# Performance work log

Measured on AMD Instinct MI355X. Metric: run time of the kernel, lower is better.

Reference implementation:

```python
import jax, jax.numpy as jnp
import numpy as np

NUM_HEADS = 12

def _get_rel_pos(q_size, k_size, rel_pos):
    # rel_pos already has shape (2*max(q,k)-1, head_dim) -> no resize needed
    q_coords = jnp.arange(q_size)[:, None] * max(k_size / q_size, 1.0)
    k_coords = jnp.arange(k_size)[None, :] * max(q_size / k_size, 1.0)
    rel = (q_coords - k_coords + (k_size - 1) * max(q_size / k_size, 1.0)).astype(jnp.int32)
    return rel_pos[rel.reshape(-1)].reshape(q_size, k_size, -1)  # (q, k, head_dim)


def setup_inputs() -> dict:
    key = jax.random.key(0)
    ks = jax.random.split(key, 7)
    B, H, W, C = 1, 64, 64, 768
    head_dim = C // NUM_HEADS
    return {
        "x": jax.random.normal(ks[0], (B, H, W, C), jnp.float32),
        "qkv_w": jax.random.normal(ks[1], (C, 3 * C), jnp.float32) * 0.02,
        "qkv_b": jax.random.normal(ks[2], (3 * C,), jnp.float32) * 0.02,
        "rel_pos_h": jax.random.normal(ks[3], (2 * H - 1, head_dim), jnp.float32) * 0.02,
        "rel_pos_w": jax.random.normal(ks[4], (2 * W - 1, head_dim), jnp.float32) * 0.02,
        "proj_w": jax.random.normal(ks[5], (C, C), jnp.float32) * 0.02,
        "proj_b": jax.random.normal(ks[6], (C,), jnp.float32) * 0.02,
    }


def reference(x, qkv_w, qkv_b, rel_pos_h, rel_pos_w, proj_w, proj_b):
    B, H, W, C = x.shape
    nh = NUM_HEADS
    hd = C // nh
    scale = hd ** (-0.5)
    S = H * W

    qkv = x @ qkv_w + qkv_b                              # (B,H,W,3C)
    qkv = qkv.reshape(B, S, 3, nh, hd).transpose(2, 0, 3, 1, 4).reshape(3, B * nh, S, hd)
    q, k, v = qkv[0], qkv[1], qkv[2]                     # (B*nh, S, hd)

    attn = jnp.einsum('bqd,bkd->bqk', q * scale, k)      # (B*nh, S, S)

    rh = _get_rel_pos(H, H, rel_pos_h)                   # (H,H,hd)
    rw = _get_rel_pos(W, W, rel_pos_w)                   # (W,W,hd)
    r_q = q.reshape(B * nh, H, W, hd)
    rel_h = jnp.einsum('bhwc,hkc->bhwk', r_q, rh)        # (B*nh,H,W,H)
    rel_w = jnp.einsum('bhwc,wkc->bhwk', r_q, rw)        # (B*nh,H,W,W)
    attn = (attn.reshape(B * nh, H, W, H, W)
            + rel_h[:, :, :, :, None]
            + rel_w[:, :, :, None, :]).reshape(B * nh, S, S)

    attn = jax.nn.softmax(attn, axis=-1)
    out = jnp.einsum('bqk,bkd->bqd', attn, v)            # (B*nh, S, hd)
    out = out.reshape(B, nh, H, W, hd).transpose(0, 2, 3, 1, 4).reshape(B, H, W, C)
    return out @ proj_w + proj_b
```

## Files before the change

kernel.cpp:

```cpp
#include <hip/hip_runtime.h>
#include <hip/hip_bf16.h>

#define S_TOK 4096
#define CDIM  768
#define N3C   2304
#define NH    12
#define HD    64

#define LOG2E 1.44269504f

typedef __attribute__((ext_vector_type(8))) short short8;
typedef __attribute__((ext_vector_type(4))) short short4v;
typedef __attribute__((ext_vector_type(4))) float float4v;
typedef __attribute__((ext_vector_type(4))) unsigned uint4v;

__device__ __forceinline__ float b2f(short s) {
    return __uint_as_float(((unsigned)(unsigned short)s) << 16);
}
__device__ __forceinline__ short f2b(float f) {
    unsigned u = __float_as_uint(f);
    unsigned r = (u + 0x7FFFu + ((u >> 16) & 1u)) >> 16;
    return (short)r;
}

#if __has_builtin(__builtin_amdgcn_exp2f)
#define EXP2F __builtin_amdgcn_exp2f
#else
#define EXP2F exp2f
#endif

__device__ __forceinline__ unsigned pack_trunc(float a, float b) {
    return __builtin_amdgcn_perm(__float_as_uint(b), __float_as_uint(a), 0x07060302u);
}

__device__ __forceinline__ short8 u4_to_s8(unsigned a, unsigned b, unsigned c, unsigned d) {
    union { uint4v u; short8 s; } t;
    t.u = (uint4v){a, b, c, d};
    return t.s;
}

__global__ __launch_bounds__(256) void cast_bf16_kernel(
    const float* __restrict__ in, short* __restrict__ out, int n4)
{
    int i = blockIdx.x * 256 + threadIdx.x;
    if (i >= n4) return;
    float4 v = ((const float4*)in)[i];
    short4v o4 = { f2b(v.x), f2b(v.y), f2b(v.z), f2b(v.w) };
    *(short4v*)&out[(size_t)i * 4] = o4;
}

__global__ __launch_bounds__(256) void transpose_cast_kernel(
    const float* __restrict__ in, short* __restrict__ out, int R, int C)
{
    __shared__ float t[64][65];
    const int tid = threadIdx.x;
    const int c0 = blockIdx.x * 64, r0 = blockIdx.y * 64;
    const int li = tid >> 6;
    const int lj = tid & 63;
#pragma unroll
    for (int p = 0; p < 16; ++p) {
        int i = p * 4 + li;
        t[i][lj] = in[(size_t)(r0 + i) * C + c0 + lj];
    }
    __syncthreads();
#pragma unroll
    for (int p = 0; p < 16; ++p) {
        int i = p * 4 + li;
        out[(size_t)(c0 + i) * R + r0 + lj] = f2b(t[lj][i]);
    }
}

#define GEMM_CORE(A_, Bt_)                                                     \
    __shared__ __align__(16) short a_s[128][72];                               \
    __shared__ __align__(16) short b_s[128][72];                               \
    const int tid  = threadIdx.x;                                              \
    const int m0 = blockIdx.y * 128;                                           \
    const int n0 = blockIdx.x * 128;                                           \
    const int lane = tid & 63, w = tid >> 6;                                   \
    const int l15 = lane & 15, quad = lane >> 4;                               \
    const int wr = w >> 1, wc = w & 1;                                         \
    const int srow = tid >> 1;                                                 \
    const int scol = (tid & 1) * 32;                                           \
    float4v acc[4][4];                                                         \
    _Pragma("unroll")                                                          \
    for (int i = 0; i < 4; ++i)                                                \
        _Pragma("unroll")                                                      \
        for (int j = 0; j < 4; ++j) acc[i][j] = (float4v){0.f,0.f,0.f,0.f};    \
    for (int k0 = 0; k0 < 768; k0 += 64) {                                     \
        __syncthreads();                                                       \
        const short* ga = A_ + (size_t)(m0 + srow) * 768 + k0 + scol;          \
        const short* gb = Bt_ + (size_t)(n0 + srow) * 768 + k0 + scol;         \
        _Pragma("unroll")                                                      \
        for (int v = 0; v < 4; ++v) {                                          \
            *(uint4*)&a_s[srow][scol + v*8] = *(const uint4*)(ga + v*8);       \
            *(uint4*)&b_s[srow][scol + v*8] = *(const uint4*)(gb + v*8);       \
        }                                                                      \
        __syncthreads();                                                       \
        _Pragma("unroll")                                                      \
        for (int kk = 0; kk < 64; kk += 32) {                                  \
            short8 af[4], bfr[4];                                              \
            _Pragma("unroll")                                                  \
            for (int i = 0; i < 4; ++i)                                        \
                af[i] = *(const short8*)&a_s[wr*64 + i*16 + l15][kk + quad*8]; \
            _Pragma("unroll")                                                  \
            for (int j = 0; j < 4; ++j)                                        \
                bfr[j] = *(const short8*)&b_s[wc*64 + j*16 + l15][kk + quad*8];\
            _Pragma("unroll")                                                  \
            for (int i = 0; i < 4; ++i)                                        \
                _Pragma("unroll")                                              \
                for (int j = 0; j < 4; ++j)                                    \
                    acc[i][j] = __builtin_amdgcn_mfma_f32_16x16x32_bf16(       \
                        af[i], bfr[j], acc[i][j], 0, 0, 0);                    \
        }                                                                      \
    }

__global__ __launch_bounds__(256) void gemm_qkv_mfma(
    const short* __restrict__ A, const short* __restrict__ Bt,
    const float* __restrict__ bias,
    short* __restrict__ Qb, short* __restrict__ Kb, short* __restrict__ Vt)
{
    GEMM_CORE(A, Bt)

    const int sec = n0 / CDIM;
    float bj[4];
#pragma unroll
    for (int j = 0; j < 4; ++j) bj[j] = bias[n0 + wc*64 + j*16 + l15];

    if (sec < 2) {
        short* dst = (sec == 0) ? Qb : Kb;
#pragma unroll
        for (int i = 0; i < 4; ++i)
#pragma unroll
            for (int j = 0; j < 4; ++j) {
                const int nn = (n0 + wc*64 + j*16 + l15) % CDIM;
                const int head = nn >> 6, d = nn & 63;
#pragma unroll
                for (int r = 0; r < 4; ++r) {
                    const int s = m0 + wr*64 + i*16 + quad*4 + r;
                    dst[((size_t)head * S_TOK + s) * HD + d] = f2b(acc[i][j][r] + bj[j]);
                }
            }
    } else {
#pragma unroll
        for (int i = 0; i < 4; ++i)
#pragma unroll
            for (int j = 0; j < 4; ++j) {
                const int nn = (n0 + wc*64 + j*16 + l15) % CDIM;
                const int head = nn >> 6, d = nn & 63;
                const int sbase = m0 + wr*64 + i*16 + quad*4;
                short4v v4;
#pragma unroll
                for (int r = 0; r < 4; ++r) v4[r] = f2b(acc[i][j][r] + bj[j]);
                *(short4v*)&Vt[((size_t)head * HD + d) * S_TOK + sbase] = v4;
            }
    }
}

__global__ __launch_bounds__(256) void gemm_proj_mfma(
    const short* __restrict__ A, const short* __restrict__ Bt,
    const float* __restrict__ bias, float* __restrict__ out)
{
    GEMM_CORE(A, Bt)

    float bj[4];
#pragma unroll
    for (int j = 0; j < 4; ++j) bj[j] = bias[n0 + wc*64 + j*16 + l15];

#pragma unroll
    for (int i = 0; i < 4; ++i)
#pragma unroll
        for (int j = 0; j < 4; ++j) {
            const int n = n0 + wc*64 + j*16 + l15;
#pragma unroll
            for (int r = 0; r < 4; ++r) {
                const int s = m0 + wr*64 + i*16 + quad*4 + r;
                out[(size_t)s * CDIM + n] = acc[i][j][r] + bj[j];
            }
        }
}

__global__ __launch_bounds__(256) void rel_mfma_kernel(
    const short* __restrict__ Qb, const float* __restrict__ rph,
    const float* __restrict__ rpw, short* __restrict__ Relh,
    short* __restrict__ Relw)
{
    __shared__ __align__(16) short q_s [64][72];
    __shared__ __align__(16) short rh_s[64][72];
    __shared__ __align__(16) short rw_s[128][72];

    const int tid  = threadIdx.x;
    const int y    = blockIdx.x;
    const int head = blockIdx.y;
    const int s0   = y * 64;
    const int w = tid >> 6, lane = tid & 63;
    const int l15 = lane & 15, quad = lane >> 4;
    const int srow = tid >> 2;
    const int scol = (tid & 3) << 4;

    {
        const uint4* g = (const uint4*)(Qb + ((size_t)head * S_TOK + s0 + srow) * HD + scol);
        *(uint4*)&q_s[srow][scol]     = g[0];
        *(uint4*)&q_s[srow][scol + 8] = g[1];
    }
    {
        const float* g = rph + (size_t)(y + srow) * HD + scol;
        short tmp[16];
#pragma unroll
        for (int i = 0; i < 16; i += 4) {
            float4 v = *(const float4*)(g + i);
            tmp[i] = f2b(v.x); tmp[i+1] = f2b(v.y); tmp[i+2] = f2b(v.z); tmp[i+3] = f2b(v.w);
        }
        *(short8*)&rh_s[srow][scol]     = *(short8*)&tmp[0];
        *(short8*)&rh_s[srow][scol + 8] = *(short8*)&tmp[8];
    }
#pragma unroll
    for (int half = 0; half < 2; ++half) {
        const int row = srow + half * 64;
        const int rr  = row > 126 ? 126 : row;
        const float* g = rpw + (size_t)rr * HD + scol;
        short tmp[16];
#pragma unroll
        for (int i = 0; i < 16; i += 4) {
            float4 v = *(const float4*)(g + i);
            tmp[i] = f2b(v.x); tmp[i+1] = f2b(v.y); tmp[i+2] = f2b(v.z); tmp[i+3] = f2b(v.w);
        }
        *(short8*)&rw_s[row][scol]     = *(short8*)&tmp[0];
        *(short8*)&rw_s[row][scol + 8] = *(short8*)&tmp[8];
    }
    __syncthreads();

    const short8 qa0 = *(const short8*)&q_s[w * 16 + l15][quad * 8];
    const short8 qa1 = *(const short8*)&q_s[w * 16 + l15][32 + quad * 8];

#pragma unroll
    for (int ct = 0; ct < 4; ++ct) {
        const int jj = ct * 16 + l15;
        short8 b0 = *(const short8*)&rh_s[jj][quad * 8];
        short8 b1 = *(const short8*)&rh_s[jj][32 + quad * 8];
        float4v z = (float4v){0.f, 0.f, 0.f, 0.f};
        z = __builtin_amdgcn_mfma_f32_16x16x32_bf16(qa0, b0, z, 0, 0, 0);
        z = __builtin_amdgcn_mfma_f32_16x16x32_bf16(qa1, b1, z, 0, 0, 0);
        const int ky = 63 - jj;
#pragma unroll
        for (int r = 0; r < 4; ++r) {
            const int q = w * 16 + quad * 4 + r;
            Relh[((size_t)head * S_TOK + s0 + q) * HD + ky] = f2b(z[r] * LOG2E);
        }
    }

#pragma unroll
    for (int ct = 0; ct < 8; ++ct) {
        const int j = ct * 16 + l15;
        short8 b0 = *(const short8*)&rw_s[j][quad * 8];
        short8 b1 = *(const short8*)&rw_s[j][32 + quad * 8];
        float4v z = (float4v){0.f, 0.f, 0.f, 0.f};
        z = __builtin_amdgcn_mfma_f32_16x16x32_bf16(qa0, b0, z, 0, 0, 0);
        z = __builtin_amdgcn_mfma_f32_16x16x32_bf16(qa1, b1, z, 0, 0, 0);
#pragma unroll
        for (int r = 0; r < 4; ++r) {
            const int q  = w * 16 + quad * 4 + r;
            const int kx = q + 63 - j;
            if (kx >= 0 && kx < 64)
                Relw[((size_t)head * S_TOK + s0 + q) * HD + kx] = f2b(z[r] * LOG2E);
        }
    }
}

__global__ __launch_bounds__(256, 3) void flash_kernel(
    const short* __restrict__ Qb, const short* __restrict__ Kb,
    const short* __restrict__ Vt, const short* __restrict__ Relh,
    const short* __restrict__ Relw, short* __restrict__ attn_b)
{
    __shared__ __align__(16) short k_s [2][64][72];
    __shared__ __align__(16) short vt_s[2][64][72];

    const int tid  = threadIdx.x;
    const int head = blockIdx.y;
    const int s0   = blockIdx.x * 64;
    const int w    = tid >> 6, lane = tid & 63;
    const int l15  = lane & 15, quad = lane >> 4;
    const int srow = tid >> 2, scol = (tid & 3) << 4;
    const int krow = (srow & 3) | (((srow >> 3) & 3) << 2)
                   | (((srow >> 2) & 1) << 4) | (srow & 32);

    const float C1 = 0.125f * LOG2E;
    const int q = w * 16 + l15;

    short8 qb0, qb1;
    {
        const short* qrow = Qb + ((size_t)head * S_TOK + s0 + q) * HD;
        qb0 = *(const short8*)(qrow + quad * 8);
        qb1 = *(const short8*)(qrow + 32 + quad * 8);
    }

    float rw[4][4];
    {
        const short* rwrow = Relw + ((size_t)head * S_TOK + s0 + q) * HD;
#pragma unroll
        for (int kt = 0; kt < 4; ++kt) {
            const int base = ((kt & 1) << 2) | ((kt >> 1) << 5);
            short4v v = *(const short4v*)(rwrow + base + quad * 8);
#pragma unroll
            for (int r = 0; r < 4; ++r) rw[kt][r] = b2f(v[r]);
        }
    }

    const short* rhrow = Relh + ((size_t)head * S_TOK + s0 + q) * HD;
    float rh_c = b2f(rhrow[0]);

    short8 aones;
#pragma unroll
    for (int j = 0; j < 8; ++j) aones[j] = (short)0x3F80;

    float4v od[4];
#pragma unroll
    for (int dt = 0; dt < 4; ++dt) od[dt] = (float4v){0.f, 0.f, 0.f, 0.f};
    float4v dq = (float4v){0.f, 0.f, 0.f, 0.f};

    const short* kbase = Kb + (size_t)head * S_TOK * HD + (size_t)srow * HD + scol;
    const short* vbase = Vt + ((size_t)head * HD + srow) * S_TOK + scol;
    {
        uint4 a = *(const uint4*)(kbase);
        uint4 b = *(const uint4*)(kbase + 8);
        uint4 c = *(const uint4*)(vbase);
        uint4 d = *(const uint4*)(vbase + 8);
        *(uint4*)&k_s[0][krow][scol]      = a;
        *(uint4*)&k_s[0][krow][scol + 8]  = b;
        *(uint4*)&vt_s[0][srow][scol]     = c;
        *(uint4*)&vt_s[0][srow][scol + 8] = d;
    }
    __syncthreads();

    for (int ic = 0; ic < 64; ++ic) {
        const int cur = ic & 1;

        uint4 pk0, pk1, pv0, pv1;
        short rhn;
        if (ic < 63) {
            const size_t ko = (size_t)(ic + 1) * 64 * HD;
            const int    vo = (ic + 1) * 64;
            pk0 = *(const uint4*)(kbase + ko);
            pk1 = *(const uint4*)(kbase + ko + 8);
            pv0 = *(const uint4*)(vbase + vo);
            pv1 = *(const uint4*)(vbase + vo + 8);
            rhn = rhrow[ic + 1];
        }

        unsigned pk[8];
#pragma unroll
        for (int kt = 0; kt < 2; ++kt) {
            const short8 ka0 = *(const short8*)&k_s[cur][kt * 16 + l15][quad * 8];
            const short8 ka1 = *(const short8*)&k_s[cur][kt * 16 + l15][32 + quad * 8];
            float4v z = (float4v){0.f, 0.f, 0.f, 0.f};
            z = __builtin_amdgcn_mfma_f32_16x16x32_bf16(ka0, qb0, z, 0, 0, 0);
            z = __builtin_amdgcn_mfma_f32_16x16x32_bf16(ka1, qb1, z, 0, 0, 0);
            float p0 = EXP2F(C1 * z[0] + (rh_c + rw[kt][0]));
            float p1 = EXP2F(C1 * z[1] + (rh_c + rw[kt][1]));
            float p2 = EXP2F(C1 * z[2] + (rh_c + rw[kt][2]));
            float p3 = EXP2F(C1 * z[3] + (rh_c + rw[kt][3]));
            pk[kt * 2]     = pack_trunc(p0, p1);
            pk[kt * 2 + 1] = pack_trunc(p2, p3);
        }
        const short8 pb0 = u4_to_s8(pk[0], pk[1], pk[2], pk[3]);

#pragma unroll
        for (int dt = 0; dt < 4; ++dt) {
            const short8 va0 = *(const short8*)&vt_s[cur][dt * 16 + l15][quad * 8];
            od[dt] = __builtin_amdgcn_mfma_f32_16x16x32_bf16(va0, pb0, od[dt], 0, 0, 0);
        }
        dq = __builtin_amdgcn_mfma_f32_16x16x32_bf16(aones, pb0, dq, 0, 0, 0);

#pragma unroll
        for (int kt = 2; kt < 4; ++kt) {
            const short8 ka0 = *(const short8*)&k_s[cur][kt * 16 + l15][quad * 8];
            const short8 ka1 = *(const short8*)&k_s[cur][kt * 16 + l15][32 + quad * 8];
            float4v z = (float4v){0.f, 0.f, 0.f, 0.f};
            z = __builtin_amdgcn_mfma_f32_16x16x32_bf16(ka0, qb0, z, 0, 0, 0);
            z = __builtin_amdgcn_mfma_f32_16x16x32_bf16(ka1, qb1, z, 0, 0, 0);
            float p0 = EXP2F(C1 * z[0] + (rh_c + rw[kt][0]));
            float p1 = EXP2F(C1 * z[1] + (rh_c + rw[kt][1]));
            float p2 = EXP2F(C1 * z[2] + (rh_c + rw[kt][2]));
            float p3 = EXP2F(C1 * z[3] + (rh_c + rw[kt][3]));
            pk[kt * 2]     = pack_trunc(p0, p1);
            pk[kt * 2 + 1] = pack_trunc(p2, p3);
        }
        const short8 pb1 = u4_to_s8(pk[4], pk[5], pk[6], pk[7]);

#pragma unroll
        for (int dt = 0; dt < 4; ++dt) {
            const short8 va1 = *(const short8*)&vt_s[cur][dt * 16 + l15][32 + quad * 8];
            od[dt] = __builtin_amdgcn_mfma_f32_16x16x32_bf16(va1, pb1, od[dt], 0, 0, 0);
        }
        dq = __builtin_amdgcn_mfma_f32_16x16x32_bf16(aones, pb1, dq, 0, 0, 0);

        if (ic < 63) {
            *(uint4*)&k_s[cur ^ 1][krow][scol]      = pk0;
            *(uint4*)&k_s[cur ^ 1][krow][scol + 8]  = pk1;
            *(uint4*)&vt_s[cur ^ 1][srow][scol]     = pv0;
            *(uint4*)&vt_s[cur ^ 1][srow][scol + 8] = pv1;
            rh_c = b2f(rhn);
            __syncthreads();
        }
    }

    const float inv = 1.f / dq[0];
    short* outp = attn_b + (size_t)(s0 + q) * CDIM + head * HD;
#pragma unroll
    for (int dt = 0; dt < 4; ++dt) {
        short4v o4;
#pragma unroll
        for (int r = 0; r < 4; ++r) o4[r] = f2b(od[dt][r] * inv);
        *(short4v*)(outp + dt * 16 + quad * 4) = o4;
    }
}

extern "C" void kernel_launch(void* const* d_in, const int* in_sizes, int n_in,
                              void* d_out, int out_size, void* d_ws, size_t ws_size,
                              hipStream_t stream)
{
    const float* x    = (const float*)d_in[0];
    const float* qkvw = (const float*)d_in[1];
    const float* qkvb = (const float*)d_in[2];
    const float* rph  = (const float*)d_in[3];
    const float* rpw  = (const float*)d_in[4];
    const float* pw   = (const float*)d_in[5];
    const float* pb   = (const float*)d_in[6];
    float* out = (float*)d_out;

    const size_t HSD = (size_t)NH * S_TOK * HD;
    short* xb     = (short*)d_ws;
    short* wt     = xb + (size_t)S_TOK * CDIM;
    short* pwt    = wt + (size_t)N3C * CDIM;
    short* Qb     = pwt + (size_t)CDIM * CDIM;
    short* Kb     = Qb + HSD;
    short* Vt     = Kb + HSD;
    short* Relh   = Vt + HSD;
    short* Relw   = Relh + HSD;
    short* attn_b = Relw + HSD;

    cast_bf16_kernel<<<S_TOK * CDIM / 4 / 256, 256, 0, stream>>>(x, xb, S_TOK * CDIM / 4);
    transpose_cast_kernel<<<dim3(N3C / 64, CDIM / 64), 256, 0, stream>>>(qkvw, wt, CDIM, N3C);
    transpose_cast_kernel<<<dim3(CDIM / 64, CDIM / 64), 256, 0, stream>>>(pw, pwt, CDIM, CDIM);

    gemm_qkv_mfma<<<dim3(N3C / 128, S_TOK / 128), 256, 0, stream>>>(
        xb, wt, qkvb, Qb, Kb, Vt);
    rel_mfma_kernel<<<dim3(64, NH), 256, 0, stream>>>(Qb, rph, rpw, Relh, Relw);
    flash_kernel<<<dim3(64, NH), 256, 0, stream>>>(Qb, Kb, Vt, Relh, Relw, attn_b);
    gemm_proj_mfma<<<dim3(CDIM / 128, S_TOK / 128), 256, 0, stream>>>(
        attn_b, pwt, pb, out);
}
```

Measured before the change: 228.4 us.

## Use direct global-to-LDS loads with XOR swizzle and two query tiles per wave

The flash kernel now runs 2 waves of 128 threads per block, each wave handling 32 query rows (two 16-row tiles), so every K/V fragment read from LDS is reused twice. K and V tiles are staged with global_load_lds straight into unpadded LDS, using an XOR swizzle to avoid bank conflicts instead of going through registers with padded rows. This cuts LDS reads and register staging per FLOP, but doubles the accumulator register footprint and leaves only 128 threads per block, which reduces occupancy and the latency hiding available to the prefetch.

Result: slower. 244.7 us (+7.2%).

```diff
diff --git a/kernel.cpp b/kernel.cpp
--- a/kernel.cpp
+++ b/kernel.cpp
@@ -37,6 +37,12 @@
     union { uint4v u; short8 s; } t;
     t.u = (uint4v){a, b, c, d};
     return t.s;
+}
+
+__device__ __forceinline__ void load_lds16(const void* g, void* l) {
+    __builtin_amdgcn_global_load_lds(
+        (const __attribute__((address_space(1))) unsigned int*)g,
+        (__attribute__((address_space(3))) unsigned int*)l, 16, 0, 0);
 }
 
 __global__ __launch_bounds__(256) void cast_bf16_kernel(
@@ -266,151 +272,171 @@
     }
 }
 
-__global__ __launch_bounds__(256, 3) void flash_kernel(
+__global__ __launch_bounds__(128, 2) void flash_kernel(
     const short* __restrict__ Qb, const short* __restrict__ Kb,
     const short* __restrict__ Vt, const short* __restrict__ Relh,
     const short* __restrict__ Relw, short* __restrict__ attn_b)
 {
-    __shared__ __align__(16) short k_s [2][64][72];
-    __shared__ __align__(16) short vt_s[2][64][72];
+    __shared__ __align__(16) short k_s [2][64][64];
+    __shared__ __align__(16) short vt_s[2][64][64];
 
     const int tid  = threadIdx.x;
     const int head = blockIdx.y;
     const int s0   = blockIdx.x * 64;
     const int w    = tid >> 6, lane = tid & 63;
     const int l15  = lane & 15, quad = lane >> 4;
-    const int srow = tid >> 2, scol = (tid & 3) << 4;
-    const int krow = (srow & 3) | (((srow >> 3) & 3) << 2)
-                   | (((srow >> 2) & 1) << 4) | (srow & 32);
 
     const float C1 = 0.125f * LOG2E;
-    const int q = w * 16 + l15;
-
-    short8 qb0, qb1;
-    {
-        const short* qrow = Qb + ((size_t)head * S_TOK + s0 + q) * HD;
-        qb0 = *(const short8*)(qrow + quad * 8);
-        qb1 = *(const short8*)(qrow + 32 + quad * 8);
-    }
-
-    float rw[4][4];
-    {
-        const short* rwrow = Relw + ((size_t)head * S_TOK + s0 + q) * HD;
+
+    const int lj = lane >> 3;
+    const int sl = (lane & 7) ^ lj;
+    const int kf = (lj & 3) + ((lj & 4) << 1) + w * 32;
+    const short* pK = Kb + (size_t)head * S_TOK * HD + (size_t)kf * HD + sl * 8;
+    const short* pV = Vt + ((size_t)head * HD + w * 32 + lj) * S_TOK + sl * 8;
+
+    const int roff0 = (quad ^ (l15 & 7)) << 4;
+    const int roff1 = roff0 ^ 64;
+
+    short8 qb[2][2];
+#pragma unroll
+    for (int qt = 0; qt < 2; ++qt) {
+        const short* qrow = Qb + ((size_t)head * S_TOK + s0 + w * 32 + qt * 16 + l15) * HD;
+        qb[qt][0] = *(const short8*)(qrow + quad * 8);
+        qb[qt][1] = *(const short8*)(qrow + 32 + quad * 8);
+    }
+
+    float rwv[2][4][4];
+#pragma unroll
+    for (int qt = 0; qt < 2; ++qt) {
+        const short* rwrow = Relw + ((size_t)head * S_TOK + s0 + w * 32 + qt * 16 + l15) * HD;
 #pragma unroll
         for (int kt = 0; kt < 4; ++kt) {
             const int base = ((kt & 1) << 2) | ((kt >> 1) << 5);
             short4v v = *(const short4v*)(rwrow + base + quad * 8);
 #pragma unroll
-            for (int r = 0; r < 4; ++r) rw[kt][r] = b2f(v[r]);
-        }
-    }
-
-    const short* rhrow = Relh + ((size_t)head * S_TOK + s0 + q) * HD;
-    float rh_c = b2f(rhrow[0]);
+            for (int r = 0; r < 4; ++r) rwv[qt][kt][r] = b2f(v[r]);
+        }
+    }
+
+    const short* rhrow0 = Relh + ((size_t)head * S_TOK + s0 + w * 32 + l15) * HD;
+    const short* rhrow1 = rhrow0 + (size_t)16 * HD;
+    float rhc0 = b2f(rhrow0[0]);
+    float rhc1 = b2f(rhrow1[0]);
 
     short8 aones;
 #pragma unroll
     for (int j = 0; j < 8; ++j) aones[j] = (short)0x3F80;
 
-    float4v od[4];
-#pragma unroll
-    for (int dt = 0; dt < 4; ++dt) od[dt] = (float4v){0.f, 0.f, 0.f, 0.f};
-    float4v dq = (float4v){0.f, 0.f, 0.f, 0.f};
-
-    const short* kbase = Kb + (size_t)head * S_TOK * HD + (size_t)srow * HD + scol;
-    const short* vbase = Vt + ((size_t)head * HD + srow) * S_TOK + scol;
+    float4v od[2][4];
+#pragma unroll
+    for (int qt = 0; qt < 2; ++qt)
+#pragma unroll
+        for (int dt = 0; dt < 4; ++dt) od[qt][dt] = (float4v){0.f, 0.f, 0.f, 0.f};
+    float4v dq0 = (float4v){0.f, 0.f, 0.f, 0.f};
+    float4v dq1 = (float4v){0.f, 0.f, 0.f, 0.f};
+
     {
-        uint4 a = *(const uint4*)(kbase);
-        uint4 b = *(const uint4*)(kbase + 8);
-        uint4 c = *(const uint4*)(vbase);
-        uint4 d = *(const uint4*)(vbase + 8);
-        *(uint4*)&k_s[0][krow][scol]      = a;
-        *(uint4*)&k_s[0][krow][scol + 8]  = b;
-        *(uint4*)&vt_s[0][srow][scol]     = c;
-        *(uint4*)&vt_s[0][srow][scol + 8] = d;
+        short* lk = &k_s[0][w * 32][0];
+        short* lv = &vt_s[0][w * 32][0];
+        load_lds16(pK,        lk);
+        load_lds16(pK + 1024, lk + 8  * 64);
+        load_lds16(pK + 256,  lk + 16 * 64);
+        load_lds16(pK + 1280, lk + 24 * 64);
+        load_lds16(pV,                      lv);
+        load_lds16(pV + 8  * S_TOK,         lv + 8  * 64);
+        load_lds16(pV + 16 * S_TOK,         lv + 16 * 64);
+        load_lds16(pV + 24 * S_TOK,         lv + 24 * 64);
     }
     __syncthreads();
 
     for (int ic = 0; ic < 64; ++ic) {
         const int cur = ic & 1;
 
-        uint4 pk0, pk1, pv0, pv1;
-        short rhn;
+        short rhn0, rhn1;
         if (ic < 63) {
-            const size_t ko = (size_t)(ic + 1) * 64 * HD;
-            const int    vo = (ic + 1) * 64;
-            pk0 = *(const uint4*)(kbase + ko);
-            pk1 = *(const uint4*)(kbase + ko + 8);
-            pv0 = *(const uint4*)(vbase + vo);
-            pv1 = *(const uint4*)(vbase + vo + 8);
-            rhn = rhrow[ic + 1];
-        }
-
-        unsigned pk[8];
-#pragma unroll
-        for (int kt = 0; kt < 2; ++kt) {
-            const short8 ka0 = *(const short8*)&k_s[cur][kt * 16 + l15][quad * 8];
-            const short8 ka1 = *(const short8*)&k_s[cur][kt * 16 + l15][32 + quad * 8];
-            float4v z = (float4v){0.f, 0.f, 0.f, 0.f};
-            z = __builtin_amdgcn_mfma_f32_16x16x32_bf16(ka0, qb0, z, 0, 0, 0);
-            z = __builtin_amdgcn_mfma_f32_16x16x32_bf16(ka1, qb1, z, 0, 0, 0);
-            float p0 = EXP2F(C1 * z[0] + (rh_c + rw[kt][0]));
-            float p1 = EXP2F(C1 * z[1] + (rh_c + rw[kt][1]));
-            float p2 = EXP2F(C1 * z[2] + (rh_c + rw[kt][2]));
-            float p3 = EXP2F(C1 * z[3] + (rh_c + rw[kt][3]));
-            pk[kt * 2]     = pack_trunc(p0, p1);
-            pk[kt * 2 + 1] = pack_trunc(p2, p3);
-        }
-        const short8 pb0 = u4_to_s8(pk[0], pk[1], pk[2], pk[3]);
+            const short* gk = pK + (ic + 1) * (64 * HD);
+            const short* gv = pV + (ic + 1) * 64;
+            short* lk = &k_s[cur ^ 1][w * 32][0];
+            short* lv = &vt_s[cur ^ 1][w * 32][0];
+            load_lds16(gk,        lk);
+            load_lds16(gk + 1024, lk + 8  * 64);
+            load_lds16(gk + 256,  lk + 16 * 64);
+            load_lds16(gk + 1280, lk + 24 * 64);
+            load_lds16(gv,              lv);
+            load_lds16(gv + 8  * S_TOK, lv + 8  * 64);
+            load_lds16(gv + 16 * S_TOK, lv + 16 * 64);
+            load_lds16(gv + 24 * S_TOK, lv + 24 * 64);
+            rhn0 = rhrow0[ic + 1];
+            rhn1 = rhrow1[ic + 1];
+        }
+
+        unsigned pkk[2][8];
+#pragma unroll
+        for (int kt = 0; kt < 4; ++kt) {
+            const char* krp = (const char*)&k_s[cur][kt * 16 + l15][0];
+            const short8 ka0 = *(const short8*)(krp + roff0);
+            const short8 ka1 = *(const short8*)(krp + roff1);
+            {
+                float4v z = (float4v){0.f, 0.f, 0.f, 0.f};
+                z = __builtin_amdgcn_mfma_f32_16x16x32_bf16(ka0, qb[0][0], z, 0, 0, 0);
+                z = __builtin_amdgcn_mfma_f32_16x16x32_bf16(ka1, qb[0][1], z, 0, 0, 0);
+                float p0 = EXP2F(C1 * z[0] + (rhc0 + rwv[0][kt][0]));
+                float p1 = EXP2F(C1 * z[1] + (rhc0 + rwv[0][kt][1]));
+                float p2 = EXP2F(C1 * z[2] + (rhc0 + rwv[0][kt][2]));
+                float p3 = EXP2F(C1 * z[3] + (rhc0 + rwv[0][kt][3]));
+                pkk[0][kt * 2]     = pack_trunc(p0, p1);
+                pkk[0][kt * 2 + 1] = pack_trunc(p2, p3);
+            }
+            {
+                float4v z = (float4v){0.f, 0.f, 0.f, 0.f};
+                z = __builtin_amdgcn_mfma_f32_16x16x32_bf16(ka0, qb[1][0], z, 0, 0, 0);
+                z = __builtin_amdgcn_mfma_f32_16x16x32_bf16(ka1, qb[1][1], z, 0, 0, 0);
+                float p0 = EXP2F(C1 * z[0] + (rhc1 + rwv[1][kt][0]));
+                float p1 = EXP2F(C1 * z[1] + (rhc1 + rwv[1][kt][1]));
+                float p2 = EXP2F(C1 * z[2] + (rhc1 + rwv[1][kt][2]));
+                float p3 = EXP2F(C1 * z[3] + (rhc1 + rwv[1][kt][3]));
+                pkk[1][kt * 2]     = pack_trunc(p0, p1);
+                pkk[1][kt * 2 + 1] = pack_trunc(p2, p3);
+            }
+        }
+        const short8 pb00 = u4_to_s8(pkk[0][0], pkk[0][1], pkk[0][2], pkk[0][3]);
+        const short8 pb01 = u4_to_s8(pkk[0][4], pkk[0][5], pkk[0][6], pkk[0][7]);
+        const short8 pb10 = u4_to_s8(pkk[1][0], pkk[1][1], pkk[1][2], pkk[1][3]);
+        const short8 pb11 = u4_to_s8(pkk[1][4], pkk[1][5], pkk[1][6], pkk[1][7]);
 
 #pragma unroll
         for (int dt = 0; dt < 4; ++dt) {
-            const short8 va0 = *(const short8*)&vt_s[cur][dt * 16 + l15][quad * 8];
-            od[dt] = __builtin_amdgcn_mfma_f32_16x16x32_bf16(va0, pb0, od[dt], 0, 0, 0);
-        }
-        dq = __builtin_amdgcn_mfma_f32_16x16x32_bf16(aones, pb0, dq, 0, 0, 0);
-
-#pragma unroll
-        for (int kt = 2; kt < 4; ++kt) {
-            const short8 ka0 = *(const short8*)&k_s[cur][kt * 16 + l15][quad * 8];
-            const short8 ka1 = *(const short8*)&k_s[cur][kt * 16 + l15][32 + quad * 8];
-            float4v z = (float4v){0.f, 0.f, 0.f, 0.f};
-            z = __builtin_amdgcn_mfma_f32_16x16x32_bf16(ka0, qb0, z, 0, 0, 0);
-            z = __builtin_amdgcn_mfma_f32_16x16x32_bf16(ka1, qb1, z, 0, 0, 0);
-            float p0 = EXP2F(C1 * z[0] + (rh_c + rw[kt][0]));
-            float p1 = EXP2F(C1 * z[1] + (rh_c + rw[kt][1]));
-            float p2 = EXP2F(C1 * z[2] + (rh_c + rw[kt][2]));
-            float p3 = EXP2F(C1 * z[3] + (rh_c + rw[kt][3]));
-            pk[kt * 2]     = pack_trunc(p0, p1);
-            pk[kt * 2 + 1] = pack_trunc(p2, p3);
-        }
-        const short8 pb1 = u4_to_s8(pk[4], pk[5], pk[6], pk[7]);
-
+            const char* vrp = (const char*)&vt_s[cur][dt * 16 + l15][0];
+            const short8 va0 = *(const short8*)(vrp + roff0);
+            const short8 va1 = *(const short8*)(vrp + roff1);
+            od[0][dt] = __builtin_amdgcn_mfma_f32_16x16x32_bf16(va0, pb00, od[0][dt], 0, 0, 0);
+            od[0][dt] = __builtin_amdgcn_mfma_f32_16x16x32_bf16(va1, pb01, od[0][dt], 0, 0, 0);
+            od[1][dt] = __builtin_amdgcn_mfma_f32_16x16x32_bf16(va0, pb10, od[1][dt], 0, 0, 0);
+            od[1][dt] = __builtin_amdgcn_mfma_f32_16x16x32_bf16(va1, pb11, od[1][dt], 0, 0, 0);
+        }
+        dq0 = __builtin_amdgcn_mfma_f32_16x16x32_bf16(aones, pb00, dq0, 0, 0, 0);
+        dq0 = __builtin_amdgcn_mfma_f32_16x16x32_bf16(aones, pb01, dq0, 0, 0, 0);
+        dq1 = __builtin_amdgcn_mfma_f32_16x16x32_bf16(aones, pb10, dq1, 0, 0, 0);
+        dq1 = __builtin_amdgcn_mfma_f32_16x16x32_bf16(aones, pb11, dq1, 0, 0, 0);
+
+        if (ic < 63) {
+            rhc0 = b2f(rhn0);
+            rhc1 = b2f(rhn1);
+            __syncthreads();
+        }
+    }
+
+#pragma unroll
+    for (int qt = 0; qt < 2; ++qt) {
+        const float inv = 1.f / ((qt == 0) ? dq0[0] : dq1[0]);
+        short* outp = attn_b + (size_t)(s0 + w * 32 + qt * 16 + l15) * CDIM + head * HD;
 #pragma unroll
         for (int dt = 0; dt < 4; ++dt) {
-            const short8 va1 = *(const short8*)&vt_s[cur][dt * 16 + l15][32 + quad * 8];
-            od[dt] = __builtin_amdgcn_mfma_f32_16x16x32_bf16(va1, pb1, od[dt], 0, 0, 0);
-        }
-        dq = __builtin_amdgcn_mfma_f32_16x16x32_bf16(aones, pb1, dq, 0, 0, 0);
-
-        if (ic < 63) {
-            *(uint4*)&k_s[cur ^ 1][krow][scol]      = pk0;
-            *(uint4*)&k_s[cur ^ 1][krow][scol + 8]  = pk1;
-            *(uint4*)&vt_s[cur ^ 1][srow][scol]     = pv0;
-            *(uint4*)&vt_s[cur ^ 1][srow][scol + 8] = pv1;
-            rh_c = b2f(rhn);
-            __syncthreads();
-        }
-    }
-
-    const float inv = 1.f / dq[0];
-    short* outp = attn_b + (size_t)(s0 + q) * CDIM + head * HD;
-#pragma unroll
-    for (int dt = 0; dt < 4; ++dt) {
-        short4v o4;
-#pragma unroll
-        for (int r = 0; r < 4; ++r) o4[r] = f2b(od[dt][r] * inv);
-        *(short4v*)(outp + dt * 16 + quad * 4) = o4;
+            short4v o4;
+#pragma unroll
+            for (int r = 0; r < 4; ++r) o4[r] = f2b(od[qt][dt][r] * inv);
+            *(short4v*)(outp + dt * 16 + quad * 4) = o4;
+        }
     }
 }
 
@@ -445,7 +471,7 @@
     gemm_qkv_mfma<<<dim3(N3C / 128, S_TOK / 128), 256, 0, stream>>>(
         xb, wt, qkvb, Qb, Kb, Vt);
     rel_mfma_kernel<<<dim3(64, NH), 256, 0, stream>>>(Qb, rph, rpw, Relh, Relw);
-    flash_kernel<<<dim3(64, NH), 256, 0, stream>>>(Qb, Kb, Vt, Relh, Relw, attn_b);
+    flash_kernel<<<dim3(64, NH), 128, 0, stream>>>(Qb, Kb, Vt, Relh, Relw, attn_b);
     gemm_proj_mfma<<<dim3(CDIM / 128, S_TOK / 128), 256, 0, stream>>>(
         attn_b, pwt, pb, out);
 }
```
